# Performance work log

Hardware: AMD Instinct MI355X
Metric: run time of the kernel (lower is better)

Reference implementation:

```python
import jax, jax.numpy as jnp
import numpy as np

CODEBOOK_SIZE = 512
LATENT_DIM = 12
BATCH = 512
TOKENS = 256


def setup_inputs() -> dict:
    key = jax.random.key(0)
    k1, k2 = jax.random.split(key)
    x = jax.random.normal(k1, (BATCH, TOKENS, LATENT_DIM), dtype=jnp.float32)
    # nn.Embedding init: uniform(-1/K, 1/K)
    lim = 1.0 / CODEBOOK_SIZE
    codebook = jax.random.uniform(k2, (CODEBOOK_SIZE, LATENT_DIM), dtype=jnp.float32,
                                  minval=-lim, maxval=lim)
    return {"x": x, "codebook": codebook}


def reference(x, codebook):
    # same as for torch.cdist (sqrt is monotonic).
    x2 = jnp.sum(x * x, axis=-1, keepdims=True)            # [B, N, 1]
    w2 = jnp.sum(codebook * codebook, axis=-1)             # [K]
    xw = jnp.einsum('bnd,kd->bnk', x, codebook)            # [B, N, K]
    dist2 = x2 - 2.0 * xw + w2                             # [B, N, K]
    indices = jnp.argmin(dist2, axis=-1)                   # [B, N] int
    quantized = codebook[indices]                          # [B, N, D]

    codebook_loss = jnp.mean((quantized - jax.lax.stop_gradient(x)) ** 2)
    commitment_loss = 0.25 * jnp.mean((jax.lax.stop_gradient(quantized) - x) ** 2)
    quantize_loss = codebook_loss + commitment_loss

    # straight-through estimator
    quantized_st = x + jax.lax.stop_gradient(quantized - x)
    return quantized_st, indices, quantize_loss
```

## Files before the change

### kernel.cpp

```cpp
#include <hip/hip_runtime.h>
#include <math.h>

namespace {
constexpr int KCB   = 512;
constexpr int DIM   = 12;
constexpr int NTOK  = 512 * 256;
constexpr int QSIZE = NTOK * DIM;
constexpr int NSPLIT = 8;
constexpr int KCHUNK = KCB / NSPLIT;
constexpr int TPT    = 2;
constexpr int TOKS_PER_BLOCK = 64 * TPT;
constexpr int NBLK   = NTOK / TOKS_PER_BLOCK;
constexpr int WVEC_FLOATS = KCB * DIM;
constexpr int CB_FLOATS   = WVEC_FLOATS + KCB;
constexpr int CB_F4       = CB_FLOATS / 4;

__global__ __launch_bounds__(256) void pack_cb(const float* __restrict__ cb,
                                               float* __restrict__ ws,
                                               float* __restrict__ out) {
    int k = blockIdx.x * blockDim.x + threadIdx.x;
    if (k == 0) out[QSIZE + NTOK] = 0.f;
    if (k >= KCB) return;
    float w[DIM];
#pragma unroll
    for (int d = 0; d < DIM; ++d) w[d] = cb[k * DIM + d];
    float w2 = 0.f;
#pragma unroll
    for (int d = 0; d < DIM; ++d) w2 += w[d] * w[d];
#pragma unroll
    for (int d = 0; d < DIM; ++d) ws[k * DIM + d] = w[d];
    ws[WVEC_FLOATS + k] = w2;
}

__device__ inline float code_score(const float (&xv)[DIM], float x2,
                                   const float4& c0, const float4& c1,
                                   const float4& c2, float w2k) {
    float xw = 0.f;
    xw = fmaf(xv[0],  c0.x, xw);
    xw = fmaf(xv[1],  c0.y, xw);
    xw = fmaf(xv[2],  c0.z, xw);
    xw = fmaf(xv[3],  c0.w, xw);
    xw = fmaf(xv[4],  c1.x, xw);
    xw = fmaf(xv[5],  c1.y, xw);
    xw = fmaf(xv[6],  c1.z, xw);
    xw = fmaf(xv[7],  c1.w, xw);
    xw = fmaf(xv[8],  c2.x, xw);
    xw = fmaf(xv[9],  c2.y, xw);
    xw = fmaf(xv[10], c2.z, xw);
    xw = fmaf(xv[11], c2.w, xw);
    return fmaf(-2.f, xw, x2) + w2k;
}

__global__ __launch_bounds__(512, 8) void vq_main(const float* __restrict__ x,
                                                  const float* __restrict__ cb,
                                                  const float* __restrict__ pk,
                                                  float* __restrict__ out) {
    __shared__ float lds[CB_FLOATS];
    const int tid  = threadIdx.x;
    const int lane = tid & 63;
    const int s = __builtin_amdgcn_readfirstlane(tid >> 6);
    const int tA = blockIdx.x * TOKS_PER_BLOCK + lane;
    const int tB = tA + 64;

    {
        float4* l4 = (float4*)lds;
        const float4* g4 = (const float4*)pk;
        for (int i = tid; i < CB_F4; i += 512) l4[i] = g4[i];
    }

    const float4* xpA = (const float4*)(x + (size_t)tA * DIM);
    const float4* xpB = (const float4*)(x + (size_t)tB * DIM);
    float4 a0 = xpA[0], a1 = xpA[1], a2 = xpA[2];
    float4 b0 = xpB[0], b1 = xpB[1], b2 = xpB[2];
    float xsA[DIM] = {a0.x, a0.y, a0.z, a0.w, a1.x, a1.y, a1.z, a1.w,
                      a2.x, a2.y, a2.z, a2.w};
    float xsB[DIM] = {b0.x, b0.y, b0.z, b0.w, b1.x, b1.y, b1.z, b1.w,
                      b2.x, b2.y, b2.z, b2.w};
    float x2A = 0.f, x2B = 0.f;
#pragma unroll
    for (int d = 0; d < DIM; ++d) x2A = fmaf(xsA[d], xsA[d], x2A);
#pragma unroll
    for (int d = 0; d < DIM; ++d) x2B = fmaf(xsB[d], xsB[d], x2B);

    __syncthreads();

    float bestA = INFINITY, bestB = INFINITY;
    int biA = 0, biB = 0;
    const int k0 = s * KCHUNK;
    const float* w2v = lds + WVEC_FLOATS;
#pragma unroll 2
    for (int g = 0; g < KCHUNK / 4; ++g) {
        float4 w2q = ((const float4*)w2v)[(k0 >> 2) + g];
        const float* cbase = lds + (size_t)(k0 + 4 * g) * DIM;
#pragma unroll
        for (int u = 0; u < 4; ++u) {
            float4 c0 = *(const float4*)(cbase + u * DIM + 0);
            float4 c1 = *(const float4*)(cbase + u * DIM + 4);
            float4 c2 = *(const float4*)(cbase + u * DIM + 8);
            float w2k = (u == 0) ? w2q.x : (u == 1) ? w2q.y : (u == 2) ? w2q.z : w2q.w;
            const int k = k0 + 4 * g + u;
            float dA = code_score(xsA, x2A, c0, c1, c2, w2k);
            float dB = code_score(xsB, x2B, c0, c1, c2, w2k);
            bool cA = dA < bestA;
            bestA = cA ? dA : bestA;
            biA   = cA ? k : biA;
            bool cB = dB < bestB;
            bestB = cB ? dB : bestB;
            biB   = cB ? k : biB;
        }
    }

    auto mkkey = [](float v, int k) {
        unsigned su = __float_as_uint(v);
        su = (su & 0x80000000u) ? ~su : (su | 0x80000000u);
        return ((unsigned long long)su << 32) | (unsigned)k;
    };
    __syncthreads();
    unsigned long long* red = (unsigned long long*)lds;
    red[s * TOKS_PER_BLOCK + lane]      = mkkey(bestA, biA);
    red[s * TOKS_PER_BLOCK + 64 + lane] = mkkey(bestB, biB);
    __syncthreads();

    if (s < TPT) {
        const int tok = s * 64 + lane;
        unsigned long long m = red[tok];
#pragma unroll
        for (int r = 1; r < NSPLIT; ++r) {
            unsigned long long v = red[r * TOKS_PER_BLOCK + tok];
            m = v < m ? v : m;
        }
        const int bid = (int)(m & 0xffffffffULL);
        unsigned eu = (unsigned)(m >> 32);
        unsigned orig = (eu & 0x80000000u) ? (eu ^ 0x80000000u) : ~eu;
        const float bsc = __uint_as_float(orig);
        const int t = blockIdx.x * TOKS_PER_BLOCK + tok;

        const float4* wrow = (const float4*)(cb + (size_t)bid * DIM);
        float4 q0 = wrow[0], q1 = wrow[1], q2 = wrow[2];
        float qs[DIM] = {q0.x, q0.y, q0.z, q0.w, q1.x, q1.y, q1.z, q1.w,
                         q2.x, q2.y, q2.z, q2.w};

        auto emit = [&](const float (&xv)[DIM]) {
            float4* qo = (float4*)(out + (size_t)t * DIM);
            float4 r0, r1, r2;
            r0.x = xv[0] + (qs[0] - xv[0]);    r0.y = xv[1] + (qs[1] - xv[1]);
            r0.z = xv[2] + (qs[2] - xv[2]);    r0.w = xv[3] + (qs[3] - xv[3]);
            r1.x = xv[4] + (qs[4] - xv[4]);    r1.y = xv[5] + (qs[5] - xv[5]);
            r1.z = xv[6] + (qs[6] - xv[6]);    r1.w = xv[7] + (qs[7] - xv[7]);
            r2.x = xv[8] + (qs[8] - xv[8]);    r2.y = xv[9] + (qs[9] - xv[9]);
            r2.z = xv[10] + (qs[10] - xv[10]); r2.w = xv[11] + (qs[11] - xv[11]);
            qo[0] = r0; qo[1] = r1; qo[2] = r2;
        };
        if (s == 0) emit(xsA); else emit(xsB);

        out[QSIZE + t] = (float)bid;

        float ls = bsc * (1.25f / (float)QSIZE);
#pragma unroll
        for (int off = 32; off > 0; off >>= 1) ls += __shfl_down(ls, off);
        if (lane == 0) atomicAdd(out + QSIZE + NTOK, ls);
    }
}
}

extern "C" void kernel_launch(void* const* d_in, const int* in_sizes, int n_in,
                              void* d_out, int out_size, void* d_ws, size_t ws_size,
                              hipStream_t stream) {
    const float* x  = (const float*)d_in[0];
    const float* cb = (const float*)d_in[1];
    float* out = (float*)d_out;
    float* pk  = (float*)d_ws;

    pack_cb<<<2, 256, 0, stream>>>(cb, pk, out);
    vq_main<<<NBLK, 512, 0, stream>>>(x, cb, pk, out);
}
```

Measured before the change: 108.4 us.

## Process eight tokens per thread to amortize codebook LDS reads

Each thread now scores eight tokens against its codebook chunk instead of two, so each LDS read of a codeword feeds eight dot products. The block covers 512 tokens, which cuts the grid size and the number of times the codebook is staged into LDS per block. The shared buffer is resized for the larger reduction table, and every wave now takes part in the final argmin merge and output write. In exchange, register pressure rises sharply (96 x values plus best scores and indices per thread), occupancy bounds drop to 2 blocks, and there are fewer blocks available to hide latency.

```diff
diff --git a/kernel.cpp b/kernel.cpp
--- a/kernel.cpp
+++ b/kernel.cpp
@@ -8,7 +8,7 @@
 constexpr int QSIZE = NTOK * DIM;
 constexpr int NSPLIT = 8;
 constexpr int KCHUNK = KCB / NSPLIT;
-constexpr int TPT    = 2;
+constexpr int TPT    = 8;
 constexpr int TOKS_PER_BLOCK = 64 * TPT;
 constexpr int NBLK   = NTOK / TOKS_PER_BLOCK;
 constexpr int WVEC_FLOATS = KCB * DIM;
@@ -51,16 +51,16 @@
     return fmaf(-2.f, xw, x2) + w2k;
 }
 
-__global__ __launch_bounds__(512, 8) void vq_main(const float* __restrict__ x,
+__global__ __launch_bounds__(512, 2) void vq_main(const float* __restrict__ x,
                                                   const float* __restrict__ cb,
                                                   const float* __restrict__ pk,
                                                   float* __restrict__ out) {
-    __shared__ float lds[CB_FLOATS];
+    __shared__ unsigned long long smem[NSPLIT * TOKS_PER_BLOCK];
+    float* lds = (float*)smem;
     const int tid  = threadIdx.x;
     const int lane = tid & 63;
     const int s = __builtin_amdgcn_readfirstlane(tid >> 6);
-    const int tA = blockIdx.x * TOKS_PER_BLOCK + lane;
-    const int tB = tA + 64;
+    const int tbase = blockIdx.x * TOKS_PER_BLOCK;
 
     {
         float4* l4 = (float4*)lds;
@@ -68,27 +68,31 @@
         for (int i = tid; i < CB_F4; i += 512) l4[i] = g4[i];
     }
 
-    const float4* xpA = (const float4*)(x + (size_t)tA * DIM);
-    const float4* xpB = (const float4*)(x + (size_t)tB * DIM);
-    float4 a0 = xpA[0], a1 = xpA[1], a2 = xpA[2];
-    float4 b0 = xpB[0], b1 = xpB[1], b2 = xpB[2];
-    float xsA[DIM] = {a0.x, a0.y, a0.z, a0.w, a1.x, a1.y, a1.z, a1.w,
-                      a2.x, a2.y, a2.z, a2.w};
-    float xsB[DIM] = {b0.x, b0.y, b0.z, b0.w, b1.x, b1.y, b1.z, b1.w,
-                      b2.x, b2.y, b2.z, b2.w};
-    float x2A = 0.f, x2B = 0.f;
+    float xs[TPT][DIM];
+    float x2[TPT];
 #pragma unroll
-    for (int d = 0; d < DIM; ++d) x2A = fmaf(xsA[d], xsA[d], x2A);
+    for (int j = 0; j < TPT; ++j) {
+        const float4* xp = (const float4*)(x + (size_t)(tbase + j * 64 + lane) * DIM);
+        float4 a0 = xp[0], a1 = xp[1], a2 = xp[2];
+        xs[j][0] = a0.x; xs[j][1] = a0.y; xs[j][2]  = a0.z; xs[j][3]  = a0.w;
+        xs[j][4] = a1.x; xs[j][5] = a1.y; xs[j][6]  = a1.z; xs[j][7]  = a1.w;
+        xs[j][8] = a2.x; xs[j][9] = a2.y; xs[j][10] = a2.z; xs[j][11] = a2.w;
+        float t2 = 0.f;
 #pragma unroll
-    for (int d = 0; d < DIM; ++d) x2B = fmaf(xsB[d], xsB[d], x2B);
+        for (int d = 0; d < DIM; ++d) t2 = fmaf(xs[j][d], xs[j][d], t2);
+        x2[j] = t2;
+    }
 
     __syncthreads();
 
-    float bestA = INFINITY, bestB = INFINITY;
-    int biA = 0, biB = 0;
+    float best[TPT];
+    int   bi[TPT];
+#pragma unroll
+    for (int j = 0; j < TPT; ++j) { best[j] = INFINITY; bi[j] = 0; }
+
     const int k0 = s * KCHUNK;
     const float* w2v = lds + WVEC_FLOATS;
-#pragma unroll 2
+#pragma unroll 1
     for (int g = 0; g < KCHUNK / 4; ++g) {
         float4 w2q = ((const float4*)w2v)[(k0 >> 2) + g];
         const float* cbase = lds + (size_t)(k0 + 4 * g) * DIM;
@@ -99,14 +103,13 @@
             float4 c2 = *(const float4*)(cbase + u * DIM + 8);
             float w2k = (u == 0) ? w2q.x : (u == 1) ? w2q.y : (u == 2) ? w2q.z : w2q.w;
             const int k = k0 + 4 * g + u;
-            float dA = code_score(xsA, x2A, c0, c1, c2, w2k);
-            float dB = code_score(xsB, x2B, c0, c1, c2, w2k);
-            bool cA = dA < bestA;
-            bestA = cA ? dA : bestA;
-            biA   = cA ? k : biA;
-            bool cB = dB < bestB;
-            bestB = cB ? dB : bestB;
-            biB   = cB ? k : biB;
+#pragma unroll
+            for (int j = 0; j < TPT; ++j) {
+                float d = code_score(xs[j], x2[j], c0, c1, c2, w2k);
+                bool c = d < best[j];
+                best[j] = c ? d : best[j];
+                bi[j]   = c ? k : bi[j];
+            }
         }
     }
 
@@ -116,42 +119,47 @@
         return ((unsigned long long)su << 32) | (unsigned)k;
     };
     __syncthreads();
-    unsigned long long* red = (unsigned long long*)lds;
-    red[s * TOKS_PER_BLOCK + lane]      = mkkey(bestA, biA);
-    red[s * TOKS_PER_BLOCK + 64 + lane] = mkkey(bestB, biB);
+#pragma unroll
+    for (int j = 0; j < TPT; ++j)
+        smem[s * TOKS_PER_BLOCK + j * 64 + lane] = mkkey(best[j], bi[j]);
     __syncthreads();
 
-    if (s < TPT) {
+    {
         const int tok = s * 64 + lane;
-        unsigned long long m = red[tok];
+        unsigned long long m = smem[tok];
 #pragma unroll
         for (int r = 1; r < NSPLIT; ++r) {
-            unsigned long long v = red[r * TOKS_PER_BLOCK + tok];
+            unsigned long long v = smem[r * TOKS_PER_BLOCK + tok];
             m = v < m ? v : m;
         }
         const int bid = (int)(m & 0xffffffffULL);
         unsigned eu = (unsigned)(m >> 32);
         unsigned orig = (eu & 0x80000000u) ? (eu ^ 0x80000000u) : ~eu;
         const float bsc = __uint_as_float(orig);
-        const int t = blockIdx.x * TOKS_PER_BLOCK + tok;
+        const int t = tbase + tok;
+
+        float xv[DIM];
+#pragma unroll
+        for (int j = 0; j < TPT; ++j)
+            if (j == s) {
+#pragma unroll
+                for (int d = 0; d < DIM; ++d) xv[d] = xs[j][d];
+            }
 
         const float4* wrow = (const float4*)(cb + (size_t)bid * DIM);
         float4 q0 = wrow[0], q1 = wrow[1], q2 = wrow[2];
         float qs[DIM] = {q0.x, q0.y, q0.z, q0.w, q1.x, q1.y, q1.z, q1.w,
                          q2.x, q2.y, q2.z, q2.w};
 
-        auto emit = [&](const float (&xv)[DIM]) {
-            float4* qo = (float4*)(out + (size_t)t * DIM);
-            float4 r0, r1, r2;
-            r0.x = xv[0] + (qs[0] - xv[0]);    r0.y = xv[1] + (qs[1] - xv[1]);
-            r0.z = xv[2] + (qs[2] - xv[2]);    r0.w = xv[3] + (qs[3] - xv[3]);
-            r1.x = xv[4] + (qs[4] - xv[4]);    r1.y = xv[5] + (qs[5] - xv[5]);
-            r1.z = xv[6] + (qs[6] - xv[6]);    r1.w = xv[7] + (qs[7] - xv[7]);
-            r2.x = xv[8] + (qs[8] - xv[8]);    r2.y = xv[9] + (qs[9] - xv[9]);
-            r2.z = xv[10] + (qs[10] - xv[10]); r2.w = xv[11] + (qs[11] - xv[11]);
-            qo[0] = r0; qo[1] = r1; qo[2] = r2;
-        };
-        if (s == 0) emit(xsA); else emit(xsB);
+        float4* qo = (float4*)(out + (size_t)t * DIM);
+        float4 r0, r1, r2;
+        r0.x = xv[0] + (qs[0] - xv[0]);    r0.y = xv[1] + (qs[1] - xv[1]);
+        r0.z = xv[2] + (qs[2] - xv[2]);    r0.w = xv[3] + (qs[3] - xv[3]);
+        r1.x = xv[4] + (qs[4] - xv[4]);    r1.y = xv[5] + (qs[5] - xv[5]);
+        r1.z = xv[6] + (qs[6] - xv[6]);    r1.w = xv[7] + (qs[7] - xv[7]);
+        r2.x = xv[8] + (qs[8] - xv[8]);    r2.y = xv[9] + (qs[9] - xv[9]);
+        r2.z = xv[10] + (qs[10] - xv[10]); r2.w = xv[11] + (qs[11] - xv[11]);
+        qo[0] = r0; qo[1] = r1; qo[2] = r2;
 
         out[QSIZE + t] = (float)bid;
 
```

Result: slower. 115.4 us (+6.4%).
